# Kernel optimization log

Measured on AMD Instinct MI355X. Metric: run time of the kernel, lower is better.

Reference implementation:

```python
import jax, jax.numpy as jnp
import numpy as np

NUM_CODEBOOKS = 8
CODEBOOK_SIZE = 2048
CODEBOOK_DIM = 16
HIDDEN_SIZE = 2048
CODEC_VOCAB_START = 0
PAD_IDX = 0


def setup_inputs() -> dict:
    key = jax.random.key(0)
    k_ids, k_emb, k_w1, k_b1, k_w2, k_b2 = jax.random.split(key, 6)
    B, S = 4, 4096
    codec_input_ids = jax.random.randint(
        k_ids, (B, S), 0, NUM_CODEBOOKS * CODEBOOK_SIZE, dtype=jnp.int64
    )
    # frozen embedding table; padding_idx row is zero
    embed_table = jax.random.normal(
        k_emb, (NUM_CODEBOOKS * CODEBOOK_SIZE, CODEBOOK_DIM), dtype=jnp.float32
    )
    embed_table = embed_table.at[PAD_IDX].set(0.0)
    # per-codebook projector params (stacked over codebook axis k)
    s1 = 1.0 / np.sqrt(CODEBOOK_DIM)
    s2 = 1.0 / np.sqrt(HIDDEN_SIZE)
    W1 = jax.random.uniform(k_w1, (NUM_CODEBOOKS, CODEBOOK_DIM, HIDDEN_SIZE), jnp.float32, -s1, s1)
    b1 = jax.random.uniform(k_b1, (NUM_CODEBOOKS, HIDDEN_SIZE), jnp.float32, -s1, s1)
    W2 = jax.random.uniform(k_w2, (NUM_CODEBOOKS, HIDDEN_SIZE, HIDDEN_SIZE), jnp.float32, -s2, s2)
    b2 = jax.random.uniform(k_b2, (NUM_CODEBOOKS, HIDDEN_SIZE), jnp.float32, -s2, s2)
    return {
        "codec_input_ids": codec_input_ids,
        "embed_table": embed_table,
        "W1": W1,
        "b1": b1,
        "W2": W2,
        "b2": b2,
    }


def reference(codec_input_ids, embed_table, W1, b1, W2, b2):
    ids = codec_input_ids - CODEC_VOCAB_START          # [B, S]
    embeds = embed_table[ids]                          # [B, S, D]
    cb = ids // CODEBOOK_SIZE                          # which codebook each token belongs to
    out = jnp.zeros(ids.shape + (HIDDEN_SIZE,), dtype=embeds.dtype)
    # fixed small loop over structurally distinct per-codebook projectors;
    # disjoint masks cover all tokens, so masked accumulation == torch scatter
    for k in range(NUM_CODEBOOKS):
        h = jnp.einsum("bsd,dh->bsh", embeds, W1[k]) + b1[k]
        h = jax.nn.gelu(h, approximate=False)          # torch nn.GELU default = exact
        h = jnp.einsum("bsh,hg->bsg", h, W2[k]) + b2[k]
        out = out + jnp.where((cb == k)[..., None], h, 0.0)
    return out
```

## Files before the change

### kernel.cpp

```cpp
#include <hip/hip_runtime.h>
#include <hip/hip_bf16.h>
#include <stdint.h>

#define NUM_CB   8
#define CB_BITS  11
#define DIM      16
#define HS       2048
#define NTOK     16384

#define BM 256
#define BN 256
#define BK 64
#define NKT (HS / BK)
#define MAXT 72

#define OFF_CUR    0u
#define OFF_NT     64u
#define OFF_GS     128u
#define OFF_TCB    256u
#define OFF_TROW   1024u
#define OFF_TVAL   2048u
#define OFF_PERM   4096u
#define OFF_H      69632u
#define OFF_W2T    67178496u
#define WS_NEED    134287360u

typedef __attribute__((ext_vector_type(8))) short s16x8;
typedef __attribute__((ext_vector_type(4))) float f32x4;

__device__ __forceinline__ void load_lds16(const void* g, const void* l) {
    __builtin_amdgcn_global_load_lds(
        (const __attribute__((address_space(1))) uint32_t*)g,
        (__attribute__((address_space(3))) uint32_t*)(void*)(uintptr_t)l, 16, 0, 0);
}

extern "C" __global__ void k_countplan(const int* __restrict__ ids,
                                       uint32_t* __restrict__ cur, uint32_t* __restrict__ numT,
                                       uint32_t* __restrict__ tcb, uint32_t* __restrict__ trow,
                                       uint32_t* __restrict__ tval, uint32_t* __restrict__ gstart) {
    __shared__ uint32_t hist[NUM_CB];
    __shared__ uint32_t s_tcb[MAXT], s_trow[MAXT], s_tval[MAXT];
    __shared__ uint32_t s_gs[NUM_CB], s_nt;
    const int tid = threadIdx.x;
    if (tid < NUM_CB) { hist[tid] = 0; cur[tid] = 0; }
    __syncthreads();
    uint32_t c0=0,c1=0,c2=0,c3=0,c4=0,c5=0,c6=0,c7=0;
    const int4* v4 = (const int4*)ids;
    for (int i = tid; i < NTOK / 4; i += 1024) {
        int4 v = v4[i];
        uint32_t a = (uint32_t)v.x >> CB_BITS, b = (uint32_t)v.y >> CB_BITS;
        uint32_t cc = (uint32_t)v.z >> CB_BITS, d = (uint32_t)v.w >> CB_BITS;
        c0 += (a==0)+(b==0)+(cc==0)+(d==0);  c1 += (a==1)+(b==1)+(cc==1)+(d==1);
        c2 += (a==2)+(b==2)+(cc==2)+(d==2);  c3 += (a==3)+(b==3)+(cc==3)+(d==3);
        c4 += (a==4)+(b==4)+(cc==4)+(d==4);  c5 += (a==5)+(b==5)+(cc==5)+(d==5);
        c6 += (a==6)+(b==6)+(cc==6)+(d==6);  c7 += (a==7)+(b==7)+(cc==7)+(d==7);
    }
    #pragma unroll
    for (int off = 32; off > 0; off >>= 1) {
        c0 += __shfl_down(c0, off); c1 += __shfl_down(c1, off);
        c2 += __shfl_down(c2, off); c3 += __shfl_down(c3, off);
        c4 += __shfl_down(c4, off); c5 += __shfl_down(c5, off);
        c6 += __shfl_down(c6, off); c7 += __shfl_down(c7, off);
    }
    if ((tid & 63) == 0) {
        if (c0) atomicAdd(&hist[0], c0); if (c1) atomicAdd(&hist[1], c1);
        if (c2) atomicAdd(&hist[2], c2); if (c3) atomicAdd(&hist[3], c3);
        if (c4) atomicAdd(&hist[4], c4); if (c5) atomicAdd(&hist[5], c5);
        if (c6) atomicAdd(&hist[6], c6); if (c7) atomicAdd(&hist[7], c7);
    }
    __syncthreads();
    if (tid == 0) {
        uint32_t ps = 0, nt = 0;
        for (int k = 0; k < NUM_CB; ++k) {
            s_gs[k] = ps;
            uint32_t c = hist[k];
            uint32_t tiles = (c + BM - 1) / BM;
            for (uint32_t m = 0; m < tiles; ++m) {
                s_tcb[nt] = (uint32_t)k;
                s_trow[nt] = ps + m * BM;
                uint32_t rem = c - m * BM;
                s_tval[nt] = rem < BM ? rem : BM;
                ++nt;
            }
            ps += c;
        }
        s_nt = nt;
    }
    __syncthreads();
    const uint32_t nt = s_nt;
    if (tid < MAXT) {
        tcb[tid]  = (tid < (int)nt) ? s_tcb[tid] : 0u;
        trow[tid] = (tid < (int)nt) ? s_trow[tid] : 0u;
        tval[tid] = (tid < (int)nt) ? s_tval[tid] : 0u;
    }
    if (tid < NUM_CB) gstart[tid] = s_gs[tid];
    if (tid == 0) *numT = nt;
}

extern "C" __global__ void k_assign(const int* __restrict__ ids, const uint32_t* __restrict__ gstart,
                                    uint32_t* __restrict__ cur, uint32_t* __restrict__ perm) {
    __shared__ uint32_t lh[NUM_CB], lbase[NUM_CB];
    const int tid = threadIdx.x;
    const int t = blockIdx.x * 256 + tid;
    if (tid < NUM_CB) lh[tid] = 0;
    __syncthreads();
    const int cb = (uint32_t)ids[t] >> CB_BITS;
    atomicAdd(&lh[cb], 1u);
    __syncthreads();
    if (tid < NUM_CB) {
        lbase[tid] = lh[tid] ? atomicAdd(&cur[tid], lh[tid]) : 0u;
        lh[tid] = 0;
    }
    __syncthreads();
    const uint32_t r = atomicAdd(&lh[cb], 1u);
    perm[gstart[cb] + lbase[cb] + r] = (uint32_t)t;
}

extern "C" __global__ void k_hbuild(const int* __restrict__ ids, const float* __restrict__ emb,
                                    const float* __restrict__ W1, const float* __restrict__ b1,
                                    const uint32_t* __restrict__ numT, const uint32_t* __restrict__ tcb,
                                    const uint32_t* __restrict__ trow, const uint32_t* __restrict__ tval,
                                    const uint32_t* __restrict__ perm, __hip_bfloat16* __restrict__ H) {
    if (blockIdx.x >= *numT) return;
    const int cb = (int)tcb[blockIdx.x];
    const int row0 = (int)trow[blockIdx.x];
    const int valid = (int)tval[blockIdx.x];
    const int col0 = blockIdx.y * 256;
    const int tid = threadIdx.x;

    __shared__ float es[BM][DIM];
    __shared__ float w1s[DIM][256];
    __shared__ int   rid[BM];

    rid[tid] = (tid < valid) ? ids[perm[row0 + tid]] : 0;
    __syncthreads();
    #pragma unroll
    for (int i = 0; i < 4; ++i) {
        int idx = i * 256 + tid;
        int r = idx >> 2, q = (idx & 3) * 4;
        *(float4*)&es[r][q] = *(const float4*)&emb[(size_t)rid[r] * DIM + q];
    }
    const float* W1k = W1 + (size_t)cb * DIM * HS + col0;
    #pragma unroll
    for (int i = 0; i < 4; ++i) {
        int idx = i * 256 + tid;
        int d = idx >> 6, c4 = (idx & 63) * 4;
        *(float4*)&w1s[d][c4] = *(const float4*)&W1k[(size_t)d * HS + c4];
    }
    __syncthreads();

    float w[DIM];
    #pragma unroll
    for (int d = 0; d < DIM; ++d) w[d] = w1s[d][tid];
    const float bb = b1[(size_t)cb * HS + col0 + tid];
    __hip_bfloat16* Hc = H + (size_t)row0 * HS + col0 + tid;

    for (int r = 0; r < BM; ++r) {
        if (r >= valid) break;
        const float4 e0 = *(const float4*)&es[r][0];
        const float4 e1 = *(const float4*)&es[r][4];
        const float4 e2 = *(const float4*)&es[r][8];
        const float4 e3 = *(const float4*)&es[r][12];
        float acc = bb;
        acc += e0.x*w[0] + e0.y*w[1] + e0.z*w[2] + e0.w*w[3];
        acc += e1.x*w[4] + e1.y*w[5] + e1.z*w[6] + e1.w*w[7];
        acc += e2.x*w[8] + e2.y*w[9] + e2.z*w[10] + e2.w*w[11];
        acc += e3.x*w[12] + e3.y*w[13] + e3.z*w[14] + e3.w*w[15];
        float g = 0.5f * acc * (1.f + erff(acc * 0.70710678118f));
        Hc[(size_t)r * HS] = __float2bfloat16(g);
    }
}

extern "C" __global__ void k_w2t(const float* __restrict__ W2, __hip_bfloat16* __restrict__ W2T) {
    __shared__ float s[64][65];
    const int k0 = blockIdx.x * 64, n0 = blockIdx.y * 64, cb = blockIdx.z;
    const int tid = threadIdx.x;
    const float* src = W2 + ((size_t)cb << 22);
    #pragma unroll
    for (int i = 0; i < 4; ++i) {
        int idx = i * 256 + tid;
        int kl = idx >> 4, n4 = (idx & 15) * 4;
        float4 v = *(const float4*)&src[(size_t)(k0 + kl) * HS + n0 + n4];
        s[kl][n4] = v.x; s[kl][n4+1] = v.y; s[kl][n4+2] = v.z; s[kl][n4+3] = v.w;
    }
    __syncthreads();
    __hip_bfloat16* dst = W2T + ((size_t)cb << 22);
    #pragma unroll
    for (int i = 0; i < 4; ++i) {
        int idx = i * 256 + tid;
        int n = idx >> 4, k4 = (idx & 15) * 4;
        __align__(8) __hip_bfloat16 o[4];
        o[0] = __float2bfloat16(s[k4+0][n]); o[1] = __float2bfloat16(s[k4+1][n]);
        o[2] = __float2bfloat16(s[k4+2][n]); o[3] = __float2bfloat16(s[k4+3][n]);
        *(ushort4*)&dst[(size_t)(n0 + n) * HS + k0 + k4] = *(const ushort4*)o;
    }
}

#define MM(m_, a_, n_, b_) acc[m_][n_] = __builtin_amdgcn_mfma_f32_16x16x32_bf16(a_, b_, acc[m_][n_], 0, 0, 0)

#define PHASE(p_, ks_, mh_, STG) do {                                          \
    const char* Ab_ = sA + (p_)*32768 + (ks_)*16384 + laneA + (mh_)*1024;      \
    const char* Bb_ = sB + (p_)*32768 + (ks_)*16384 + laneB;                   \
    s16x8 a0 = *(const s16x8*)(Ab_);                                           \
    s16x8 a1 = *(const s16x8*)(Ab_ + 256);                                     \
    s16x8 a2 = *(const s16x8*)(Ab_ + 512);                                     \
    s16x8 a3 = *(const s16x8*)(Ab_ + 768);                                     \
    s16x8 bb0 = *(const s16x8*)(Bb_);                                          \
    s16x8 bb1 = *(const s16x8*)(Bb_ + 256);                                    \
    s16x8 bb2 = *(const s16x8*)(Bb_ + 512);                                    \
    s16x8 bb3 = *(const s16x8*)(Bb_ + 768);                                    \
    STG;                                                                       \
    __builtin_amdgcn_s_barrier();                                              \
    asm volatile("s_waitcnt lgkmcnt(0)" ::: "memory");                         \
    __builtin_amdgcn_sched_barrier(0);                                         \
    __builtin_amdgcn_s_setprio(1);                                             \
    MM((mh_)*4+0, a0, 0, bb0); MM((mh_)*4+0, a0, 1, bb1);                      \
    MM((mh_)*4+0, a0, 2, bb2); MM((mh_)*4+0, a0, 3, bb3);                      \
    MM((mh_)*4+1, a1, 0, bb0); MM((mh_)*4+1, a1, 1, bb1);                      \
    MM((mh_)*4+1, a1, 2, bb2); MM((mh_)*4+1, a1, 3, bb3);                      \
    MM((mh_)*4+2, a2, 0, bb0); MM((mh_)*4+2, a2, 1, bb1);                      \
    MM((mh_)*4+2, a2, 2, bb2); MM((mh_)*4+2, a2, 3, bb3);                      \
    MM((mh_)*4+3, a3, 0, bb0); MM((mh_)*4+3, a3, 1, bb1);                      \
    MM((mh_)*4+3, a3, 2, bb2); MM((mh_)*4+3, a3, 3, bb3);                      \
    __builtin_amdgcn_s_setprio(0);                                             \
} while (0)

#define STAGE_A(q_, c47_, koff_) do {                                          \
    const unsigned short* _g = gA_t + (koff_) + (c47_) * 32;                   \
    load_lds16(_g,      sA + (q_)*32768 + (c47_)*16384 + wbase);               \
    load_lds16(_g + 16, sA + (q_)*32768 + (c47_)*16384 + wbase + 8192);        \
} while (0)
#define STAGE_B(q_, c47_, koff_) do {                                          \
    const unsigned short* _g = gB_t + (koff_) + (c47_) * 32;                   \
    load_lds16(_g,      sB + (q_)*32768 + (c47_)*16384 + wbase);               \
    load_lds16(_g + 16, sB + (q_)*32768 + (c47_)*16384 + wbase + 8192);        \
} while (0)

#define VM4 asm volatile("s_waitcnt vmcnt(4)" ::: "memory")
#define VM0 asm volatile("s_waitcnt vmcnt(0)" ::: "memory")
#define BAR __builtin_amdgcn_s_barrier()
#define NOSTG ((void)0)

extern "C" __global__ void __launch_bounds__(512, 2) k_gemm(
    const __hip_bfloat16* __restrict__ Hb, const __hip_bfloat16* __restrict__ W2Tb,
    const float* __restrict__ b2, const uint32_t* __restrict__ numT,
    const uint32_t* __restrict__ tcb, const uint32_t* __restrict__ trow,
    const uint32_t* __restrict__ tval, const uint32_t* __restrict__ perm,
    float* __restrict__ out)
{
    const int mslot = blockIdx.y;
    if (mslot >= (int)*numT) return;
    const int cb = (int)tcb[mslot];
    const int row0 = (int)trow[mslot];
    const int valid = (int)tval[mslot];
    const int n0 = blockIdx.x * BN;

    const int tid = threadIdx.x;
    const int lane = tid & 63, wave = tid >> 6;
    const int wm = wave >> 2, wn = wave & 3;

    __shared__ __align__(16) char sA[65536];
    __shared__ __align__(16) char sB[65536];

    const unsigned short* H  = (const unsigned short*)Hb;
    const unsigned short* W2 = (const unsigned short*)W2Tb;

    const int trl = tid & 255;
    const int rA = trl < valid ? trl : (valid - 1);
    const unsigned short* gA_t = H  + (size_t)(row0 + rA) * HS + (tid >> 8) * 8;
    const unsigned short* gB_t = W2 + ((size_t)cb * HS + n0 + trl) * HS + (tid >> 8) * 8;
    const uint32_t wbase = (uint32_t)__builtin_amdgcn_readfirstlane((uint32_t)(wave << 10));

    const uint32_t laneA = ((uint32_t)(lane >> 4) << 12) + (((uint32_t)(lane & 15) + wm * 128) << 4);
    const uint32_t laneB = ((uint32_t)(lane >> 4) << 12) + (((uint32_t)(lane & 15) + wn * 64) << 4);

    f32x4 acc[8][4];
    #pragma unroll
    for (int i = 0; i < 8; ++i)
        #pragma unroll
        for (int j = 0; j < 4; ++j) acc[i][j] = (f32x4){0.f, 0.f, 0.f, 0.f};

    STAGE_A(0, 0, 0); STAGE_B(0, 0, 0); STAGE_A(0, 1, 0); STAGE_B(0, 1, 0);
    VM4;
    BAR;

    #pragma unroll 2
    for (int kt = 0; kt < NKT - 1; ++kt) {
        const int p = kt & 1, q = p ^ 1;
        const int koff = (kt + 1) * BK;
        PHASE(p, 0, 0, STAGE_A(q, 0, koff));      BAR;
        PHASE(p, 0, 1, STAGE_B(q, 0, koff)); VM4; BAR;
        PHASE(p, 1, 0, STAGE_A(q, 1, koff));      BAR;
        PHASE(p, 1, 1, STAGE_B(q, 1, koff)); VM4; BAR;
    }
    PHASE(1, 0, 0, NOSTG);      BAR;
    PHASE(1, 0, 1, NOSTG); VM0; BAR;
    PHASE(1, 1, 0, NOSTG);      BAR;
    PHASE(1, 1, 1, NOSTG);

    const float* b2k = b2 + (size_t)cb * HS;
    const int colb = n0 + wn * 64 + (lane & 15);
    float bias[4];
    #pragma unroll
    for (int nf = 0; nf < 4; ++nf) bias[nf] = b2k[colb + nf * 16];

    #pragma unroll
    for (int mf = 0; mf < 8; ++mf) {
        #pragma unroll
        for (int jj = 0; jj < 4; ++jj) {
            const int m = wm * 128 + mf * 16 + (lane >> 4) * 4 + jj;
            if (m < valid) {
                float* op = out + (size_t)perm[row0 + m] * HS;
                #pragma unroll
                for (int nf = 0; nf < 4; ++nf)
                    op[colb + nf * 16] = acc[mf][nf][jj] + bias[nf];
            }
        }
    }
}

extern "C" void kernel_launch(void* const* d_in, const int* in_sizes, int n_in,
                              void* d_out, int out_size, void* d_ws, size_t ws_size,
                              hipStream_t stream) {
    const int*   ids = (const int*)d_in[0];
    const float* emb = (const float*)d_in[1];
    const float* W1  = (const float*)d_in[2];
    const float* b1  = (const float*)d_in[3];
    const float* W2  = (const float*)d_in[4];
    const float* b2  = (const float*)d_in[5];
    float* out = (float*)d_out;

    if (ws_size < (size_t)WS_NEED) return;

    char* ws = (char*)d_ws;
    uint32_t* cur    = (uint32_t*)(ws + OFF_CUR);
    uint32_t* numT   = (uint32_t*)(ws + OFF_NT);
    uint32_t* gstart = (uint32_t*)(ws + OFF_GS);
    uint32_t* tcb    = (uint32_t*)(ws + OFF_TCB);
    uint32_t* trow   = (uint32_t*)(ws + OFF_TROW);
    uint32_t* tval   = (uint32_t*)(ws + OFF_TVAL);
    uint32_t* perm   = (uint32_t*)(ws + OFF_PERM);
    __hip_bfloat16* Hbf  = (__hip_bfloat16*)(ws + OFF_H);
    __hip_bfloat16* W2Tb = (__hip_bfloat16*)(ws + OFF_W2T);

    k_countplan<<<1, 1024, 0, stream>>>(ids, cur, numT, tcb, trow, tval, gstart);
    k_assign   <<<NTOK / 256, 256, 0, stream>>>(ids, gstart, cur, perm);
    k_w2t      <<<dim3(32, 32, 8), 256, 0, stream>>>(W2, W2Tb);
    k_hbuild   <<<dim3(MAXT, 8), 256, 0, stream>>>(ids, emb, W1, b1, numT, tcb, trow, tval, perm, Hbf);
    k_gemm     <<<dim3(HS / BN, MAXT), 512, 0, stream>>>(Hbf, W2Tb, b2, numT, tcb, trow, tval, perm, out);
}
```

Baseline: 650.5 us.

## Reuse B fragments across M halves and remap GEMM grid for XCD locality

```diff
diff --git a/kernel.cpp b/kernel.cpp
--- a/kernel.cpp
+++ b/kernel.cpp
@@ -13,6 +13,7 @@
 #define BK 64
 #define NKT (HS / BK)
 #define MAXT 72
+#define GEMM_GRID (8 * MAXT)
 
 #define OFF_CUR    0u
 #define OFF_NT     64u
@@ -198,33 +199,6 @@
 
 #define MM(m_, a_, n_, b_) acc[m_][n_] = __builtin_amdgcn_mfma_f32_16x16x32_bf16(a_, b_, acc[m_][n_], 0, 0, 0)
 
-#define PHASE(p_, ks_, mh_, STG) do {                                          \
-    const char* Ab_ = sA + (p_)*32768 + (ks_)*16384 + laneA + (mh_)*1024;      \
-    const char* Bb_ = sB + (p_)*32768 + (ks_)*16384 + laneB;                   \
-    s16x8 a0 = *(const s16x8*)(Ab_);                                           \
-    s16x8 a1 = *(const s16x8*)(Ab_ + 256);                                     \
-    s16x8 a2 = *(const s16x8*)(Ab_ + 512);                                     \
-    s16x8 a3 = *(const s16x8*)(Ab_ + 768);                                     \
-    s16x8 bb0 = *(const s16x8*)(Bb_);                                          \
-    s16x8 bb1 = *(const s16x8*)(Bb_ + 256);                                    \
-    s16x8 bb2 = *(const s16x8*)(Bb_ + 512);                                    \
-    s16x8 bb3 = *(const s16x8*)(Bb_ + 768);                                    \
-    STG;                                                                       \
-    __builtin_amdgcn_s_barrier();                                              \
-    asm volatile("s_waitcnt lgkmcnt(0)" ::: "memory");                         \
-    __builtin_amdgcn_sched_barrier(0);                                         \
-    __builtin_amdgcn_s_setprio(1);                                             \
-    MM((mh_)*4+0, a0, 0, bb0); MM((mh_)*4+0, a0, 1, bb1);                      \
-    MM((mh_)*4+0, a0, 2, bb2); MM((mh_)*4+0, a0, 3, bb3);                      \
-    MM((mh_)*4+1, a1, 0, bb0); MM((mh_)*4+1, a1, 1, bb1);                      \
-    MM((mh_)*4+1, a1, 2, bb2); MM((mh_)*4+1, a1, 3, bb3);                      \
-    MM((mh_)*4+2, a2, 0, bb0); MM((mh_)*4+2, a2, 1, bb1);                      \
-    MM((mh_)*4+2, a2, 2, bb2); MM((mh_)*4+2, a2, 3, bb3);                      \
-    MM((mh_)*4+3, a3, 0, bb0); MM((mh_)*4+3, a3, 1, bb1);                      \
-    MM((mh_)*4+3, a3, 2, bb2); MM((mh_)*4+3, a3, 3, bb3);                      \
-    __builtin_amdgcn_s_setprio(0);                                             \
-} while (0)
-
 #define STAGE_A(q_, c47_, koff_) do {                                          \
     const unsigned short* _g = gA_t + (koff_) + (c47_) * 32;                   \
     load_lds16(_g,      sA + (q_)*32768 + (c47_)*16384 + wbase);               \
@@ -239,7 +213,42 @@
 #define VM4 asm volatile("s_waitcnt vmcnt(4)" ::: "memory")
 #define VM0 asm volatile("s_waitcnt vmcnt(0)" ::: "memory")
 #define BAR __builtin_amdgcn_s_barrier()
+#define LGK0 asm volatile("s_waitcnt lgkmcnt(0)" ::: "memory")
+#define SCHB __builtin_amdgcn_sched_barrier(0)
 #define NOSTG ((void)0)
+
+#define PHASE_B(p_, ks_, STG) do {                                             \
+    const char* Bb_ = sB + (p_)*32768 + (ks_)*16384 + laneB;                   \
+    bb0 = *(const s16x8*)(Bb_);       bb1 = *(const s16x8*)(Bb_ + 256);        \
+    bb2 = *(const s16x8*)(Bb_ + 512); bb3 = *(const s16x8*)(Bb_ + 768);        \
+    const char* Ab_ = sA + (p_)*32768 + (ks_)*16384 + laneA;                   \
+    s16x8 a0 = *(const s16x8*)(Ab_);       s16x8 a1 = *(const s16x8*)(Ab_ + 256); \
+    s16x8 a2 = *(const s16x8*)(Ab_ + 512); s16x8 a3 = *(const s16x8*)(Ab_ + 768); \
+    STG;                                                                       \
+    __builtin_amdgcn_s_barrier();                                              \
+    LGK0; SCHB;                                                                \
+    __builtin_amdgcn_s_setprio(1);                                             \
+    MM(0, a0, 0, bb0); MM(0, a0, 1, bb1); MM(0, a0, 2, bb2); MM(0, a0, 3, bb3);\
+    MM(1, a1, 0, bb0); MM(1, a1, 1, bb1); MM(1, a1, 2, bb2); MM(1, a1, 3, bb3);\
+    MM(2, a2, 0, bb0); MM(2, a2, 1, bb1); MM(2, a2, 2, bb2); MM(2, a2, 3, bb3);\
+    MM(3, a3, 0, bb0); MM(3, a3, 1, bb1); MM(3, a3, 2, bb2); MM(3, a3, 3, bb3);\
+    __builtin_amdgcn_s_setprio(0);                                             \
+} while (0)
+
+#define PHASE_R(p_, ks_, STG) do {                                             \
+    const char* Ab_ = sA + (p_)*32768 + (ks_)*16384 + laneA + 1024;            \
+    s16x8 a0 = *(const s16x8*)(Ab_);       s16x8 a1 = *(const s16x8*)(Ab_ + 256); \
+    s16x8 a2 = *(const s16x8*)(Ab_ + 512); s16x8 a3 = *(const s16x8*)(Ab_ + 768); \
+    STG;                                                                       \
+    __builtin_amdgcn_s_barrier();                                              \
+    LGK0; SCHB;                                                                \
+    __builtin_amdgcn_s_setprio(1);                                             \
+    MM(4, a0, 0, bb0); MM(4, a0, 1, bb1); MM(4, a0, 2, bb2); MM(4, a0, 3, bb3);\
+    MM(5, a1, 0, bb0); MM(5, a1, 1, bb1); MM(5, a1, 2, bb2); MM(5, a1, 3, bb3);\
+    MM(6, a2, 0, bb0); MM(6, a2, 1, bb1); MM(6, a2, 2, bb2); MM(6, a2, 3, bb3);\
+    MM(7, a3, 0, bb0); MM(7, a3, 1, bb1); MM(7, a3, 2, bb2); MM(7, a3, 3, bb3);\
+    __builtin_amdgcn_s_setprio(0);                                             \
+} while (0)
 
 extern "C" __global__ void __launch_bounds__(512, 2) k_gemm(
     const __hip_bfloat16* __restrict__ Hb, const __hip_bfloat16* __restrict__ W2Tb,
@@ -248,12 +257,14 @@
     const uint32_t* __restrict__ tval, const uint32_t* __restrict__ perm,
     float* __restrict__ out)
 {
-    const int mslot = blockIdx.y;
+    const int wg = (int)(blockIdx.x & 7) * (GEMM_GRID / 8) + (int)(blockIdx.x >> 3);
+    const int mslot = wg >> 3;
+    const int nb = wg & 7;
     if (mslot >= (int)*numT) return;
     const int cb = (int)tcb[mslot];
     const int row0 = (int)trow[mslot];
     const int valid = (int)tval[mslot];
-    const int n0 = blockIdx.x * BN;
+    const int n0 = nb * BN;
 
     const int tid = threadIdx.x;
     const int lane = tid & 63, wave = tid >> 6;
@@ -280,23 +291,24 @@
         #pragma unroll
         for (int j = 0; j < 4; ++j) acc[i][j] = (f32x4){0.f, 0.f, 0.f, 0.f};
 
+    s16x8 bb0, bb1, bb2, bb3;
+
     STAGE_A(0, 0, 0); STAGE_B(0, 0, 0); STAGE_A(0, 1, 0); STAGE_B(0, 1, 0);
     VM4;
     BAR;
 
-    #pragma unroll 2
     for (int kt = 0; kt < NKT - 1; ++kt) {
         const int p = kt & 1, q = p ^ 1;
         const int koff = (kt + 1) * BK;
-        PHASE(p, 0, 0, STAGE_A(q, 0, koff));      BAR;
-        PHASE(p, 0, 1, STAGE_B(q, 0, koff)); VM4; BAR;
-        PHASE(p, 1, 0, STAGE_A(q, 1, koff));      BAR;
-        PHASE(p, 1, 1, STAGE_B(q, 1, koff)); VM4; BAR;
-    }
-    PHASE(1, 0, 0, NOSTG);      BAR;
-    PHASE(1, 0, 1, NOSTG); VM0; BAR;
-    PHASE(1, 1, 0, NOSTG);      BAR;
-    PHASE(1, 1, 1, NOSTG);
+        PHASE_B(p, 0, STAGE_A(q, 0, koff));      BAR;
+        PHASE_R(p, 0, STAGE_B(q, 0, koff)); VM4; BAR;
+        PHASE_B(p, 1, STAGE_A(q, 1, koff));      BAR;
+        PHASE_R(p, 1, STAGE_B(q, 1, koff)); VM4; BAR;
+    }
+    PHASE_B(1, 0, NOSTG);      BAR;
+    PHASE_R(1, 0, NOSTG); VM0; BAR;
+    PHASE_B(1, 1, NOSTG);      BAR;
+    PHASE_R(1, 1, NOSTG);
 
     const float* b2k = b2 + (size_t)cb * HS;
     const int colb = n0 + wn * 64 + (lane & 15);
@@ -347,5 +359,5 @@
     k_assign   <<<NTOK / 256, 256, 0, stream>>>(ids, gstart, cur, perm);
     k_w2t      <<<dim3(32, 32, 8), 256, 0, stream>>>(W2, W2Tb);
     k_hbuild   <<<dim3(MAXT, 8), 256, 0, stream>>>(ids, emb, W1, b1, numT, tcb, trow, tval, perm, Hbf);
-    k_gemm     <<<dim3(HS / BN, MAXT), 512, 0, stream>>>(Hbf, W2Tb, b2, numT, tcb, trow, tval, perm, out);
-}
+    k_gemm     <<<GEMM_GRID, 512, 0, stream>>>(Hbf, W2Tb, b2, numT, tcb, trow, tval, perm, out);
+}
```

New measurement: 635.2 us. 2.4% less time.
